# Kernel optimization log

Measured on AMD Instinct MI355X. Metric: run time of the kernel, lower is better.

Reference implementation:

```python
import jax, jax.numpy as jnp
import numpy as np

B, CIN, HID, HEADS, K, STRIDE, PAD, W = 8, 256, 256, 8, 31, 1, 15, 16384
HD = HID // HEADS  # head dim
DN = ('NCHW', 'OIHW', 'NCHW')


def setup_inputs() -> dict:
    key = jax.random.key(0)
    ks = jax.random.split(key, 6)
    std = 1.0 / np.sqrt(HD)
    return dict(
        x=jax.random.normal(ks[0], (B, CIN, 1, W), jnp.float32),
        query=(jax.random.normal(ks[1], (HID,), jnp.float32) * std),
        Wk=(jax.random.normal(ks[2], (CIN, HID), jnp.float32) * std),
        Wk_bias=jnp.zeros((HID,), jnp.float32),
        rpe=0.02 * jax.random.normal(ks[3], (HEADS, 1, 1, K), jnp.float32),
        to_v_w=(jax.random.normal(ks[4], (HID, CIN, 1, 1), jnp.float32) / np.sqrt(CIN)),
        to_v_b=jnp.zeros((HID,), jnp.float32),
        to_out_w=(jax.random.normal(ks[5], (HID, HID, 1, 1), jnp.float32) / np.sqrt(HID)),
        to_out_b=jnp.zeros((HID,), jnp.float32),
    )


def reference(x, query, Wk, Wk_bias, rpe, to_v_w, to_v_b, to_out_w, to_out_b):
    Bsz = x.shape[0]
    # shared learned query -> [B, heads, hd], normalized and scaled
    q = jnp.broadcast_to(query, (Bsz, HID)).reshape(Bsz, HEADS, HD)
    q = q / (jnp.linalg.norm(q, axis=-1, keepdims=True) + 1e-6)
    q = q / np.sqrt(HD)
    # fused QK: (q @ Wk^T) @ x  -> cost [B, heads, 1, W]
    Wk_r = Wk.reshape(CIN, HEADS, HD)
    qWk = jnp.einsum('bhd,Dhd->bDh', q, Wk_r)          # [B, CIN, heads]
    cost = jnp.einsum('bDhw,bDc->bchw', x, qWk)        # [B, heads, 1, W]
    qWk_b = jnp.einsum('hd,bhd->bh', Wk_bias.reshape(HEADS, HD), q)
    cost = cost + qWk_b[:, :, None, None]
    cost_exp = jnp.exp(cost)
    # v = 1x1 conv (to_v)
    v = jnp.einsum('bdhw,od->bohw', x, to_v_w.reshape(HID, CIN)) + to_v_b[None, :, None, None]
    # exp-weighted values, grouped windowed sums
    vc = (cost_exp[:, :, None] * v.reshape(Bsz, HEADS, HD, 1, W)).reshape(Bsz, HID, 1, W)
    rpe_exp = jnp.exp(rpe)                             # [heads, 1, 1, K]
    kern_v = jnp.repeat(rpe_exp, HD, axis=0)           # [HID, 1, 1, K] depthwise
    sum_v = jax.lax.conv_general_dilated(
        vc, kern_v, (1, STRIDE), ((0, 0), (PAD, PAD)),
        feature_group_count=HID, dimension_numbers=DN)
    sum_c = jax.lax.conv_general_dilated(
        cost_exp, rpe_exp, (1, STRIDE), ((0, 0), (PAD, PAD)),
        feature_group_count=HEADS, dimension_numbers=DN)
    Wo = sum_v.shape[-1]
    out = sum_v.reshape(Bsz, HEADS, HD, 1, Wo) / sum_c.reshape(Bsz, HEADS, 1, 1, Wo)
    out = out.reshape(Bsz, HID, 1, Wo)
    # to_out 1x1 conv
    out = jnp.einsum('bdhw,od->bohw', out, to_out_w.reshape(HID, HID)) + to_out_b[None, :, None, None]
    return out
```

## Files before the change

kernel.cpp:

```cpp
#include <hip/hip_runtime.h>
#include <hip/hip_bf16.h>
#include <math.h>

#define BATCH  8
#define NHEADS 8
#define KW     31
#define W      16384

#define WS_QWKB 2048
#define WS_RPE  2056
#define OFF_WVH 9216
#define OFF_WOH (OFF_WVH + 131072)
#define OFF_CE  (OFF_WOH + 131072)

typedef __attribute__((ext_vector_type(8))) short  short8;
typedef __attribute__((ext_vector_type(4))) float  f32x4;

__device__ __forceinline__ float f4c(const float4& v, int i) {
  switch (i) { case 0: return v.x; case 1: return v.y; case 2: return v.z; default: return v.w; }
}
__device__ __forceinline__ unsigned short f2bf(float f) {
  union { __hip_bfloat16 h; unsigned short u; } cv; cv.h = __float2bfloat16(f); return cv.u;
}
__device__ __forceinline__ float bf2f(unsigned short u) {
  union { __hip_bfloat16 h; unsigned short u; } cv; cv.u = u; return __bfloat162float(cv.h);
}

__global__ __launch_bounds__(256) void prep_kernel(
    const float* __restrict__ query, const float* __restrict__ Wk,
    const float* __restrict__ Wkb, const float* __restrict__ rpe,
    const float* __restrict__ Wv, const float* __restrict__ Wo,
    float* __restrict__ ws, unsigned short* __restrict__ WvH,
    unsigned short* __restrict__ WoH) {
  int t = threadIdx.x, bid = blockIdx.x;
  if (bid == 0) {
    __shared__ float q_l[256];
    float qv = query[t];
    float ss = qv * qv;
    #pragma unroll
    for (int m = 16; m >= 1; m >>= 1) ss += __shfl_xor(ss, m, 32);
    qv = qv / (sqrtf(ss) + 1e-6f) * 0.17677669529663687f;
    q_l[t] = qv;
    __syncthreads();
    const float* wr = Wk + (size_t)t * 256;
    #pragma unroll
    for (int h = 0; h < 8; ++h) {
      float s = 0.f;
      #pragma unroll
      for (int d = 0; d < 32; ++d) s = fmaf(q_l[h*32 + d], wr[h*32 + d], s);
      ws[t*8 + h] = s;
    }
    float pb = Wkb[t] * q_l[t];
    #pragma unroll
    for (int m = 16; m >= 1; m >>= 1) pb += __shfl_xor(pb, m, 32);
    if ((t & 31) == 0) ws[WS_QWKB + (t >> 5)] = pb;
    if (t < NHEADS * KW) ws[WS_RPE + t] = __expf(rpe[t]);
  } else {
    const float* src = (bid <= 4) ? Wv : Wo;
    unsigned short* dst = (bid <= 4) ? WvH : WoH;
    int seg = (bid - 1) & 3;
    int base4 = seg * 4096;
    #pragma unroll
    for (int it = 0; it < 16; ++it) {
      int i4 = base4 + t + 256 * it;
      float4 v = ((const float4*)src)[i4];
      ushort4 o;
      o.x = f2bf(v.x); o.y = f2bf(v.y); o.z = f2bf(v.z); o.w = f2bf(v.w);
      ((ushort4*)dst)[i4] = o;
    }
  }
}

__global__ __launch_bounds__(512, 4) void xv_kernel(
    const float* __restrict__ x, const float* __restrict__ wsf,
    const unsigned short* __restrict__ A,
    const float* __restrict__ bias,
    float* __restrict__ ceout, float* __restrict__ vcout, int b0) {
  __shared__ float xs[64 * 260];
  __shared__ float cbuf[4 * 576];
  __shared__ float ceL[512];
  __shared__ float biasL[256];

  int t = threadIdx.x;
  int bb = blockIdx.y, b = b0 + bb;
  int w0 = blockIdx.x * 64;
  if (t < 256) biasL[t] = bias[t];

  {
    int tt = t & 255, db2 = t >> 8;
    int rr = tt >> 4, c2 = tt & 15;
    #pragma unroll
    for (int dd = 0; dd < 2; ++dd) {
      int db = db2 * 2 + dd;
      float4 v0 = *(const float4*)(x + ((size_t)b*256 + db*64 + rr*4 + 0)*W + w0 + c2*4);
      float4 v1 = *(const float4*)(x + ((size_t)b*256 + db*64 + rr*4 + 1)*W + w0 + c2*4);
      float4 v2 = *(const float4*)(x + ((size_t)b*256 + db*64 + rr*4 + 2)*W + w0 + c2*4);
      float4 v3 = *(const float4*)(x + ((size_t)b*256 + db*64 + rr*4 + 3)*W + w0 + c2*4);
      #pragma unroll
      for (int i = 0; i < 4; ++i) {
        float4 tv = make_float4(f4c(v0,i), f4c(v1,i), f4c(v2,i), f4c(v3,i));
        *(float4*)&xs[(c2*4 + i)*260 + db*64 + rr*4] = tv;
      }
    }
  }
  __syncthreads();

  int w = t & 63, q = t >> 6;
  int qu = __builtin_amdgcn_readfirstlane(q);

  f32x4 xr[8];
  {
    const float* xrow = &xs[w*260 + qu*32];
    #pragma unroll
    for (int i = 0; i < 8; ++i) xr[i] = *(const f32x4*)(xrow + 4*i);
    float ca[8] = {0,0,0,0,0,0,0,0};
    const float* qkb = wsf + (size_t)qu*256;
    #pragma unroll
    for (int k4 = 0; k4 < 8; ++k4) {
      const float* qr = qkb + k4*32;
      #pragma unroll
      for (int e = 0; e < 4; ++e) {
        #pragma unroll
        for (int h = 0; h < 8; ++h)
          ca[h] = fmaf(xr[k4][e], qr[e*8 + h], ca[h]);
      }
    }
    if (q < 4) {
      #pragma unroll
      for (int h = 0; h < 8; ++h) cbuf[q*576 + w*9 + h] = ca[h];
    } else {
      #pragma unroll
      for (int h = 0; h < 8; ++h) xr[h & 7][0] = xr[h & 7][0];
      #pragma unroll
      for (int h = 0; h < 8; ++h) {  asm volatile("" :: "v"(ca[h])); }
    }
    __syncthreads();

    {
      unsigned short* hrow = (unsigned short*)xs + w*520 + qu*32;
      #pragma unroll
      for (int kc = 0; kc < 4; ++kc) {
        short8 hs, ls;
        #pragma unroll
        for (int e = 0; e < 4; ++e) {
          float a0 = xr[2*kc][e], a1 = xr[2*kc+1][e];
          unsigned short h0 = f2bf(a0), h1 = f2bf(a1);
          hs[e]   = (short)h0;  hs[e+4] = (short)h1;
          ls[e]   = (short)f2bf(a0 - bf2f(h0));
          ls[e+4] = (short)f2bf(a1 - bf2f(h1));
        }
        *(short8*)(hrow + 8*kc)       = hs;
        *(short8*)(hrow + 256 + 8*kc) = ls;
      }
    }
    float acc0;
    {
      int hR = t >> 6 & 7, wR = t & 63;
      acc0 = cbuf[0*576 + wR*9 + hR] + cbuf[1*576 + wR*9 + hR]
           + cbuf[2*576 + wR*9 + hR] + cbuf[3*576 + wR*9 + hR];
    }
    __syncthreads();
    if (q >= 4) {
      #pragma unroll
      for (int h = 0; h < 8; ++h) cbuf[(q-4)*576 + w*9 + h] = ca[h];
    }
    __syncthreads();

    {
      int hR = t >> 6 & 7, wR = t & 63;
      float sum = acc0 + cbuf[0*576 + wR*9 + hR] + cbuf[1*576 + wR*9 + hR]
                + cbuf[2*576 + wR*9 + hR] + cbuf[3*576 + wR*9 + hR]
                + wsf[WS_QWKB + hR];
      float ce = __expf(sum);
      ceL[hR*64 + wR] = ce;
      ceout[((size_t)bb*8 + hR)*W + w0 + wR] = ce;
    }
  }
  __syncthreads();

  int wid = t >> 6, quad = (t >> 4) & 3, m = t & 15;
  f32x4 acc[2][4];
  #pragma unroll
  for (int j = 0; j < 2; ++j)
    #pragma unroll
    for (int c = 0; c < 4; ++c) acc[j][c] = (f32x4){0.f, 0.f, 0.f, 0.f};

  const unsigned short* xsu = (const unsigned short*)xs;
  #pragma unroll
  for (int kk = 0; kk < 8; ++kk) {
    int ko = kk*32 + quad*8;
    short8 a0 = *(const short8*)(A + (size_t)(32*wid + m)*256 + ko);
    short8 a1 = *(const short8*)(A + (size_t)(32*wid + 16 + m)*256 + ko);
    #pragma unroll
    for (int c = 0; c < 4; ++c) {
      int rw = 16*c + m;
      short8 bh = *(const short8*)(xsu + rw*520 + ko);
      short8 bl = *(const short8*)(xsu + rw*520 + 256 + ko);
      acc[0][c] = __builtin_amdgcn_mfma_f32_16x16x32_bf16(a0, bh, acc[0][c], 0, 0, 0);
      acc[0][c] = __builtin_amdgcn_mfma_f32_16x16x32_bf16(a0, bl, acc[0][c], 0, 0, 0);
      acc[1][c] = __builtin_amdgcn_mfma_f32_16x16x32_bf16(a1, bh, acc[1][c], 0, 0, 0);
      acc[1][c] = __builtin_amdgcn_mfma_f32_16x16x32_bf16(a1, bl, acc[1][c], 0, 0, 0);
    }
  }
  __syncthreads();

  #pragma unroll
  for (int j = 0; j < 2; ++j) {
    int ob = 32*wid + 16*j + 4*quad;
    #pragma unroll
    for (int c = 0; c < 4; ++c) {
      int wc = 16*c + m;
      float ce = ceL[wid*64 + wc];
      f32x4 r;
      #pragma unroll
      for (int i = 0; i < 4; ++i) r[i] = (acc[j][c][i] + biasL[ob + i]) * ce;
      *(f32x4*)(xs + wc*260 + ob) = r;
    }
  }
  __syncthreads();
  {
    float* vg = vcout + ((size_t)bb*W + w0)*256;
    #pragma unroll
    for (int it = 0; it < 8; ++it) {
      int idx = t + 512*it;
      int row = idx >> 6, c4 = (idx & 63)*4;
      f32x4 v = *(const f32x4*)(xs + row*260 + c4);
      *(f32x4*)(vg + (size_t)idx*4) = v;
    }
  }
}

__global__ __launch_bounds__(256, 4) void conv_kernel(
    const float* __restrict__ vc, const float* __restrict__ costexp,
    const float* __restrict__ rpe_ws, unsigned short* __restrict__ u) {
  __shared__ float vcl[94 * 68];
  __shared__ float cel[2 * 96];
  __shared__ float rcl[2 * 64];
  __shared__ float rpel[2 * 32];

  int t = threadIdx.x;
  int qd = blockIdx.y, bb = blockIdx.z;
  int w0 = blockIdx.x * 64;
  int h0 = qd * 2;

  if (t < 64) rpel[t] = ((t & 31) < KW) ? rpe_ws[(h0 + (t >> 5))*KW + (t & 31)] : 0.f;
  if (t < 192) {
    int h2 = t / 96, c = t % 96;
    int gw = w0 - 15 + c;
    cel[t] = (c < 94 && gw >= 0 && gw < W) ? costexp[((size_t)bb*8 + h0 + h2)*W + gw] : 0.f;
  }
  #pragma unroll
  for (int it = 0; it < 6; ++it) {
    int idx = t + 256*it;
    int r = idx >> 4, c4 = (idx & 15)*4;
    if (r < 94) {
      int gw = w0 - 15 + r;
      float4 v = make_float4(0.f, 0.f, 0.f, 0.f);
      if (gw >= 0 && gw < W)
        v = *(const float4*)(vc + ((size_t)bb*W + gw)*256 + qd*64 + c4);
      *(float4*)&vcl[r*68 + c4] = v;
    }
  }
  __syncthreads();

  if (t < 128) {
    int h2 = t >> 6, w = t & 63;
    float acc = 0.f;
    #pragma unroll
    for (int k = 0; k < KW; ++k) acc = fmaf(rpel[h2*32 + k], cel[h2*96 + w + k], acc);
    rcl[h2*64 + w] = 1.0f / acc;
  }
  __syncthreads();

  int p = t & 31, g = t >> 5;
  int h2 = p >> 4;
  float rp[KW];
  #pragma unroll
  for (int k = 0; k < KW; ++k) rp[k] = rpel[h2*32 + k];

  float ax[8], ay[8];
  #pragma unroll
  for (int i = 0; i < 8; ++i) { ax[i] = 0.f; ay[i] = 0.f; }
  #pragma unroll
  for (int s = 0; s < 38; ++s) {
    float2 v = *(const float2*)&vcl[(8*g + s)*68 + 2*p];
    #pragma unroll
    for (int i = 0; i < 8; ++i) {
      int k = s - i;
      if (k >= 0 && k < KW) {
        ax[i] = fmaf(rp[k], v.x, ax[i]);
        ay[i] = fmaf(rp[k], v.y, ay[i]);
      }
    }
  }
  #pragma unroll
  for (int i = 0; i < 8; ++i) {
    int o = 8*g + i;
    float rc = rcl[h2*64 + o];
    float ux = ax[i] * rc, uy = ay[i] * rc;
    unsigned short hx = f2bf(ux), hy = f2bf(uy);
    unsigned short lx = f2bf(ux - bf2f(hx)), ly = f2bf(uy - bf2f(hy));
    unsigned short* ud = u + ((size_t)bb*W + w0 + o)*512 + qd*64 + 2*p;
    ushort2 hvv; hvv.x = hx; hvv.y = hy;
    ushort2 lvv; lvv.x = lx; lvv.y = ly;
    *(ushort2*)(ud)       = hvv;
    *(ushort2*)(ud + 256) = lvv;
  }
}

__global__ __launch_bounds__(256, 4) void gemm_out(
    const unsigned short* __restrict__ A, const float* __restrict__ bias,
    const unsigned short* __restrict__ u, float* __restrict__ outp, int b0) {
  __shared__ unsigned short bs[64 * 264];
  __shared__ float biasL[256];

  int t = threadIdx.x;
  int bb = blockIdx.y;
  int w0 = blockIdx.x * 64;
  biasL[t] = bias[t];

  int wid = t >> 6, quad = (t >> 4) & 3, m = t & 15;
  f32x4 acc[4][4];
  #pragma unroll
  for (int j = 0; j < 4; ++j)
    #pragma unroll
    for (int c = 0; c < 4; ++c) acc[j][c] = (f32x4){0.f, 0.f, 0.f, 0.f};

  const unsigned short* src = u + ((size_t)bb*W + w0)*512;
  #pragma unroll
  for (int pass = 0; pass < 2; ++pass) {
    #pragma unroll
    for (int it = 0; it < 8; ++it) {
      int idx = t + 256*it;
      int row = idx >> 5, cc = (idx & 31)*8;
      *(short8*)(bs + row*264 + cc) =
          *(const short8*)(src + (size_t)row*512 + pass*256 + cc);
    }
    __syncthreads();
    #pragma unroll
    for (int kk = 0; kk < 8; ++kk) {
      int ko = kk*32 + quad*8;
      short8 a[4];
      #pragma unroll
      for (int j = 0; j < 4; ++j)
        a[j] = *(const short8*)(A + (size_t)(64*wid + 16*j + m)*256 + ko);
      #pragma unroll
      for (int c = 0; c < 4; ++c) {
        short8 bv = *(const short8*)(bs + (16*c + m)*264 + ko);
        #pragma unroll
        for (int j = 0; j < 4; ++j)
          acc[j][c] = __builtin_amdgcn_mfma_f32_16x16x32_bf16(a[j], bv, acc[j][c], 0, 0, 0);
      }
    }
    __syncthreads();
  }

  float* og = outp + (size_t)(b0 + bb)*256*W;
  #pragma unroll
  for (int j = 0; j < 4; ++j) {
    int ob = 64*wid + 16*j + 4*quad;
    #pragma unroll
    for (int c = 0; c < 4; ++c) {
      int w = w0 + 16*c + m;
      #pragma unroll
      for (int i = 0; i < 4; ++i)
        og[(size_t)(ob + i)*W + w] = acc[j][c][i] + biasL[ob + i];
    }
  }
}

extern "C" void kernel_launch(void* const* d_in, const int* in_sizes, int n_in,
                              void* d_out, int out_size, void* d_ws, size_t ws_size,
                              hipStream_t stream) {
  const float* x     = (const float*)d_in[0];
  const float* query = (const float*)d_in[1];
  const float* Wk    = (const float*)d_in[2];
  const float* Wkb   = (const float*)d_in[3];
  const float* rpe   = (const float*)d_in[4];
  const float* Wv    = (const float*)d_in[5];
  const float* tvb   = (const float*)d_in[6];
  const float* Wo    = (const float*)d_in[7];
  const float* tob   = (const float*)d_in[8];
  float* out = (float*)d_out;
  char* wsb  = (char*)d_ws;
  float* wsf = (float*)d_ws;

  unsigned short* WvH = (unsigned short*)(wsb + OFF_WVH);
  unsigned short* WoH = (unsigned short*)(wsb + OFF_WOH);

  const size_t per_b = (size_t)8*W*4 + (size_t)W*256*4 + (size_t)W*512*2;
  int NB = (int)((ws_size > OFF_CE) ? ((ws_size - OFF_CE) / per_b) : 1);
  if (NB > BATCH) NB = BATCH;
  if (NB < 1) NB = 1;

  float*          ceB = (float*)(wsb + OFF_CE);
  float*          vcB = (float*)(wsb + OFF_CE + (size_t)NB*8*W*4);
  unsigned short* uB  = (unsigned short*)(wsb + OFF_CE + (size_t)NB*8*W*4 + (size_t)NB*W*256*4);

  prep_kernel<<<9, 256, 0, stream>>>(query, Wk, Wkb, rpe, Wv, Wo, wsf, WvH, WoH);

  for (int b0 = 0; b0 < BATCH; b0 += NB) {
    int nb = (BATCH - b0 < NB) ? (BATCH - b0) : NB;
    xv_kernel<<<dim3(256, nb), 512, 0, stream>>>(x, wsf, WvH, tvb, ceB, vcB, b0);
    conv_kernel<<<dim3(256, 4, nb), 256, 0, stream>>>(vcB, ceB, wsf + WS_RPE, uB);
    gemm_out<<<dim3(256, nb), 256, 0, stream>>>(WoH, tob, uB, out, b0);
  }
}
```

Measured before the change: 472.8 us.

## Fuse windowed conv and output GEMM into one kernel via shared memory

Merges the depthwise windowed-sum kernel and the to_out GEMM into a single kernel per 32-column tile. The bf16 hi/lo split of the normalized values stays in LDS instead of round-tripping a large u buffer through global memory, and output stores are staged through LDS for coalesced writes. Tile blocks are also remapped with a swizzle. In exchange the conv recomputes halo loads per head slice with many syncs, and the smaller 32-wide tile gives less MFMA reuse of the A weights per block.

```diff
diff --git a/kernel.cpp b/kernel.cpp
--- a/kernel.cpp
+++ b/kernel.cpp
@@ -130,9 +130,7 @@
       for (int h = 0; h < 8; ++h) cbuf[q*576 + w*9 + h] = ca[h];
     } else {
       #pragma unroll
-      for (int h = 0; h < 8; ++h) xr[h & 7][0] = xr[h & 7][0];
-      #pragma unroll
-      for (int h = 0; h < 8; ++h) {  asm volatile("" :: "v"(ca[h])); }
+      for (int h = 0; h < 8; ++h) { asm volatile("" :: "v"(ca[h])); }
     }
     __syncthreads();
 
@@ -230,141 +228,122 @@
   }
 }
 
-__global__ __launch_bounds__(256, 4) void conv_kernel(
+__global__ __launch_bounds__(512, 6) void cg_kernel(
     const float* __restrict__ vc, const float* __restrict__ costexp,
-    const float* __restrict__ rpe_ws, unsigned short* __restrict__ u) {
-  __shared__ float vcl[94 * 68];
-  __shared__ float cel[2 * 96];
-  __shared__ float rcl[2 * 64];
-  __shared__ float rpel[2 * 32];
+    const float* __restrict__ rpe_ws, const unsigned short* __restrict__ A,
+    const float* __restrict__ bias, float* __restrict__ outp, int b0) {
+  __shared__ __align__(16) float vcl[62 * 36];
+  __shared__ __align__(16) unsigned short ubuf[2][32*264];
+  __shared__ float cel[8 * 64];
+  __shared__ float rcl[8 * 32];
+  __shared__ float rpel[8 * 32];
+  __shared__ float biasL[256];
 
   int t = threadIdx.x;
-  int qd = blockIdx.y, bb = blockIdx.z;
-  int w0 = blockIdx.x * 64;
-  int h0 = qd * 2;
-
-  if (t < 64) rpel[t] = ((t & 31) < KW) ? rpe_ws[(h0 + (t >> 5))*KW + (t & 31)] : 0.f;
-  if (t < 192) {
-    int h2 = t / 96, c = t % 96;
-    int gw = w0 - 15 + c;
-    cel[t] = (c < 94 && gw >= 0 && gw < W) ? costexp[((size_t)bb*8 + h0 + h2)*W + gw] : 0.f;
-  }
-  #pragma unroll
-  for (int it = 0; it < 6; ++it) {
-    int idx = t + 256*it;
-    int r = idx >> 4, c4 = (idx & 15)*4;
-    if (r < 94) {
+  int bb = blockIdx.y;
+  int tx = blockIdx.x;
+  int tile = ((tx & 7) << 6) | (tx >> 3);
+  int w0 = tile * 32;
+
+  if (t < 256) {
+    biasL[t] = bias[t];
+    int h = t >> 5, k = t & 31;
+    rpel[t] = (k < KW) ? rpe_ws[h*KW + k] : 0.f;
+  }
+  {
+    int h = t >> 6, c = t & 63;
+    if (c < 62) {
+      int gw = w0 - 15 + c;
+      cel[h*64 + c] = (gw >= 0 && gw < W) ? costexp[((size_t)bb*8 + h)*W + gw] : 0.f;
+    }
+  }
+  __syncthreads();
+  if (t < 256) {
+    int h = t >> 5, w = t & 31;
+    float acc = 0.f;
+    #pragma unroll
+    for (int k = 0; k < KW; ++k) acc = fmaf(rpel[h*32 + k], cel[h*64 + w + k], acc);
+    rcl[t] = 1.0f / acc;
+  }
+
+  int wv = t >> 4, p = t & 15;
+  for (int q = 0; q < 8; ++q) {
+    if (t < 496) {
+      int r = t >> 3, c4 = (t & 7) * 4;
       int gw = w0 - 15 + r;
       float4 v = make_float4(0.f, 0.f, 0.f, 0.f);
       if (gw >= 0 && gw < W)
-        v = *(const float4*)(vc + ((size_t)bb*W + gw)*256 + qd*64 + c4);
-      *(float4*)&vcl[r*68 + c4] = v;
-    }
-  }
-  __syncthreads();
-
-  if (t < 128) {
-    int h2 = t >> 6, w = t & 63;
-    float acc = 0.f;
-    #pragma unroll
-    for (int k = 0; k < KW; ++k) acc = fmaf(rpel[h2*32 + k], cel[h2*96 + w + k], acc);
-    rcl[h2*64 + w] = 1.0f / acc;
-  }
-  __syncthreads();
-
-  int p = t & 31, g = t >> 5;
-  int h2 = p >> 4;
-  float rp[KW];
-  #pragma unroll
-  for (int k = 0; k < KW; ++k) rp[k] = rpel[h2*32 + k];
-
-  float ax[8], ay[8];
-  #pragma unroll
-  for (int i = 0; i < 8; ++i) { ax[i] = 0.f; ay[i] = 0.f; }
-  #pragma unroll
-  for (int s = 0; s < 38; ++s) {
-    float2 v = *(const float2*)&vcl[(8*g + s)*68 + 2*p];
-    #pragma unroll
-    for (int i = 0; i < 8; ++i) {
-      int k = s - i;
-      if (k >= 0 && k < KW) {
-        ax[i] = fmaf(rp[k], v.x, ax[i]);
-        ay[i] = fmaf(rp[k], v.y, ay[i]);
-      }
-    }
-  }
-  #pragma unroll
-  for (int i = 0; i < 8; ++i) {
-    int o = 8*g + i;
-    float rc = rcl[h2*64 + o];
-    float ux = ax[i] * rc, uy = ay[i] * rc;
-    unsigned short hx = f2bf(ux), hy = f2bf(uy);
-    unsigned short lx = f2bf(ux - bf2f(hx)), ly = f2bf(uy - bf2f(hy));
-    unsigned short* ud = u + ((size_t)bb*W + w0 + o)*512 + qd*64 + 2*p;
-    ushort2 hvv; hvv.x = hx; hvv.y = hy;
-    ushort2 lvv; lvv.x = lx; lvv.y = ly;
-    *(ushort2*)(ud)       = hvv;
-    *(ushort2*)(ud + 256) = lvv;
-  }
-}
-
-__global__ __launch_bounds__(256, 4) void gemm_out(
-    const unsigned short* __restrict__ A, const float* __restrict__ bias,
-    const unsigned short* __restrict__ u, float* __restrict__ outp, int b0) {
-  __shared__ unsigned short bs[64 * 264];
-  __shared__ float biasL[256];
-
-  int t = threadIdx.x;
-  int bb = blockIdx.y;
-  int w0 = blockIdx.x * 64;
-  biasL[t] = bias[t];
+        v = *(const float4*)(vc + ((size_t)bb*W + gw)*256 + q*32 + c4);
+      *(float4*)&vcl[r*36 + c4] = v;
+    }
+    __syncthreads();
+    {
+      float ax = 0.f, ay = 0.f;
+      #pragma unroll
+      for (int k = 0; k < KW; ++k) {
+        float rpk = rpel[q*32 + k];
+        float2 v = *(const float2*)&vcl[(wv + k)*36 + 2*p];
+        ax = fmaf(rpk, v.x, ax);
+        ay = fmaf(rpk, v.y, ay);
+      }
+      float rc = rcl[q*32 + wv];
+      float ux = ax * rc, uy = ay * rc;
+      unsigned short hx = f2bf(ux), hy = f2bf(uy);
+      unsigned short lx = f2bf(ux - bf2f(hx)), ly = f2bf(uy - bf2f(hy));
+      ushort2 hv; hv.x = hx; hv.y = hy;
+      ushort2 lv; lv.x = lx; lv.y = ly;
+      *(ushort2*)&ubuf[0][wv*264 + q*32 + 2*p] = hv;
+      *(ushort2*)&ubuf[1][wv*264 + q*32 + 2*p] = lv;
+    }
+    __syncthreads();
+  }
 
   int wid = t >> 6, quad = (t >> 4) & 3, m = t & 15;
-  f32x4 acc[4][4];
-  #pragma unroll
-  for (int j = 0; j < 4; ++j)
-    #pragma unroll
-    for (int c = 0; c < 4; ++c) acc[j][c] = (f32x4){0.f, 0.f, 0.f, 0.f};
-
-  const unsigned short* src = u + ((size_t)bb*W + w0)*512;
+  f32x4 acc[2][2];
+  #pragma unroll
+  for (int j = 0; j < 2; ++j)
+    #pragma unroll
+    for (int c = 0; c < 2; ++c) acc[j][c] = (f32x4){0.f, 0.f, 0.f, 0.f};
+
   #pragma unroll
   for (int pass = 0; pass < 2; ++pass) {
-    #pragma unroll
-    for (int it = 0; it < 8; ++it) {
-      int idx = t + 256*it;
-      int row = idx >> 5, cc = (idx & 31)*8;
-      *(short8*)(bs + row*264 + cc) =
-          *(const short8*)(src + (size_t)row*512 + pass*256 + cc);
-    }
-    __syncthreads();
+    const unsigned short* bsrc = ubuf[pass];
     #pragma unroll
     for (int kk = 0; kk < 8; ++kk) {
       int ko = kk*32 + quad*8;
-      short8 a[4];
-      #pragma unroll
-      for (int j = 0; j < 4; ++j)
-        a[j] = *(const short8*)(A + (size_t)(64*wid + 16*j + m)*256 + ko);
-      #pragma unroll
-      for (int c = 0; c < 4; ++c) {
-        short8 bv = *(const short8*)(bs + (16*c + m)*264 + ko);
-        #pragma unroll
-        for (int j = 0; j < 4; ++j)
-          acc[j][c] = __builtin_amdgcn_mfma_f32_16x16x32_bf16(a[j], bv, acc[j][c], 0, 0, 0);
-      }
-    }
-    __syncthreads();
-  }
-
-  float* og = outp + (size_t)(b0 + bb)*256*W;
-  #pragma unroll
-  for (int j = 0; j < 4; ++j) {
-    int ob = 64*wid + 16*j + 4*quad;
-    #pragma unroll
-    for (int c = 0; c < 4; ++c) {
-      int w = w0 + 16*c + m;
+      short8 a0 = *(const short8*)(A + (size_t)(32*wid + m)*256 + ko);
+      short8 a1 = *(const short8*)(A + (size_t)(32*wid + 16 + m)*256 + ko);
+      #pragma unroll
+      for (int c = 0; c < 2; ++c) {
+        short8 bv = *(const short8*)(bsrc + (16*c + m)*264 + ko);
+        acc[0][c] = __builtin_amdgcn_mfma_f32_16x16x32_bf16(a0, bv, acc[0][c], 0, 0, 0);
+        acc[1][c] = __builtin_amdgcn_mfma_f32_16x16x32_bf16(a1, bv, acc[1][c], 0, 0, 0);
+      }
+    }
+  }
+  __syncthreads();
+
+  float* outs = (float*)ubuf;
+  #pragma unroll
+  for (int j = 0; j < 2; ++j) {
+    int ob = 32*wid + 16*j + 4*quad;
+    #pragma unroll
+    for (int c = 0; c < 2; ++c) {
+      int w = 16*c + m;
       #pragma unroll
       for (int i = 0; i < 4; ++i)
-        og[(size_t)(ob + i)*W + w] = acc[j][c][i] + biasL[ob + i];
+        outs[(ob + i)*32 + w] = acc[j][c][i] + biasL[ob + i];
+    }
+  }
+  __syncthreads();
+  {
+    float* og = outp + (size_t)(b0 + bb)*256*W + w0;
+    #pragma unroll
+    for (int it = 0; it < 4; ++it) {
+      int idx = t + 512*it;
+      int o = idx >> 3, c4 = (idx & 7)*4;
+      f32x4 v = *(const f32x4*)(outs + o*32 + c4);
+      *(f32x4*)(og + (size_t)o*W + c4) = v;
     }
   }
 }
@@ -388,21 +367,19 @@
   unsigned short* WvH = (unsigned short*)(wsb + OFF_WVH);
   unsigned short* WoH = (unsigned short*)(wsb + OFF_WOH);
 
-  const size_t per_b = (size_t)8*W*4 + (size_t)W*256*4 + (size_t)W*512*2;
+  const size_t per_b = (size_t)8*W*4 + (size_t)W*256*4;
   int NB = (int)((ws_size > OFF_CE) ? ((ws_size - OFF_CE) / per_b) : 1);
   if (NB > BATCH) NB = BATCH;
   if (NB < 1) NB = 1;
 
-  float*          ceB = (float*)(wsb + OFF_CE);
-  float*          vcB = (float*)(wsb + OFF_CE + (size_t)NB*8*W*4);
-  unsigned short* uB  = (unsigned short*)(wsb + OFF_CE + (size_t)NB*8*W*4 + (size_t)NB*W*256*4);
+  float* ceB = (float*)(wsb + OFF_CE);
+  float* vcB = (float*)(wsb + OFF_CE + (size_t)NB*8*W*4);
 
   prep_kernel<<<9, 256, 0, stream>>>(query, Wk, Wkb, rpe, Wv, Wo, wsf, WvH, WoH);
 
   for (int b0 = 0; b0 < BATCH; b0 += NB) {
     int nb = (BATCH - b0 < NB) ? (BATCH - b0) : NB;
     xv_kernel<<<dim3(256, nb), 512, 0, stream>>>(x, wsf, WvH, tvb, ceB, vcB, b0);
-    conv_kernel<<<dim3(256, 4, nb), 256, 0, stream>>>(vcB, ceB, wsf + WS_RPE, uB);
-    gemm_out<<<dim3(256, nb), 256, 0, stream>>>(WoH, tob, uB, out, b0);
-  }
-}
+    cg_kernel<<<dim3(512, nb), 512, 0, stream>>>(vcB, ceB, wsf + WS_RPE, WoH, tob, out, b0);
+  }
+}
```

Result: no change. 469.1 us (-0.8%).
